# Optimization experiments

Measured on AMD Instinct MI355X. Metric: run time of the kernel, lower is better.

The kernel has to match this reference:

```python
import jax, jax.numpy as jnp
import numpy as np

DIM = 2048
HID = 4096          # multiple_of*ceil(int(2*6144/3)/256)
STATE = 128
HEADS = 64
GROUPS = 1
CONV = 4
CHUNK = 256
HEAD_DIM = HID // HEADS            # 64
CONV_DIM = HID + 2 * GROUPS * STATE  # 4352
D_IN = 2 * HID + 2 * GROUPS * STATE + HEADS  # 8512


def setup_inputs() -> dict:
    key = jax.random.key(0)
    ks = jax.random.split(key, 8)
    x = jax.random.normal(ks[0], (1, 4096, DIM), dtype=jnp.float32)
    in_proj_w = jax.random.normal(ks[1], (D_IN, DIM), jnp.float32) * (DIM ** -0.5)
    conv_w = jax.random.normal(ks[2], (CONV_DIM, CONV), jnp.float32) * (CONV ** -0.5)
    # dt_bias init: log(expm1(uniform(dt_min, dt_max)))
    dt_bias = jnp.log(jnp.expm1(jax.random.uniform(ks[3], (HEADS,), jnp.float32, 0.001, 0.1)))
    # A_log init: log(uniform(A_init_min, A_init_max))
    A_log = jnp.log(jax.random.uniform(ks[4], (HEADS,), jnp.float32, 1.0, 16.0))
    D = jnp.ones((HEADS,), jnp.float32)
    norm_w = jnp.ones((HID,), jnp.float32)
    out_proj_w = jax.random.normal(ks[5], (DIM, HID), jnp.float32) * (HID ** -0.5)
    return dict(x=x, in_proj_w=in_proj_w, conv_w=conv_w, dt_bias=dt_bias,
                A_log=A_log, D=D, norm_w=norm_w, out_proj_w=out_proj_w)


def _causal_conv1d_silu(xBC, w):
    # xBC: (b, s, c); w: (c, k) depthwise causal conv, then SiLU
    b, s, c = xBC.shape
    k = w.shape[1]
    xp = jnp.pad(xBC, ((0, 0), (k - 1, 0), (0, 0)))
    out = xp[:, 0:s, :] * w[:, 0]
    for i in range(1, k):
        out = out + xp[:, i:i + s, :] * w[:, i]
    return jax.nn.silu(out)


def _ssd_chunk_scan(x, dt, A, B, C, D, chunk):
    # x: (b,s,h,p), dt: (b,s,h) post-softplus, A: (h,) negative, B,C: (b,s,g,n)
    b, s, h, p = x.shape
    g, n = B.shape[2], B.shape[3]
    c = s // chunk
    Bh = jnp.repeat(B, h // g, axis=2).reshape(b, c, chunk, h, n)
    Ch = jnp.repeat(C, h // g, axis=2).reshape(b, c, chunk, h, n)
    xr = x.reshape(b, c, chunk, h, p)
    dtr = dt.reshape(b, c, chunk, h)
    dA = dtr * A                      # (b,c,l,h)
    dAc = jnp.cumsum(dA, axis=2)      # (b,c,l,h)
    # intra-chunk (diagonal blocks): decay[i,j] = exp(dAc[i]-dAc[j]) for i>=j
    seg = dAc[:, :, :, None, :] - dAc[:, :, None, :, :]   # (b,c,l,l,h)
    mask = jnp.tril(jnp.ones((chunk, chunk), bool))
    Lmat = jnp.where(mask[None, None, :, :, None], jnp.exp(seg), 0.0)
    xdt = xr * dtr[..., None]         # dt-scaled inputs
    y_diag = jnp.einsum('bclhn,bcshn,bclsh,bcshp->bclhp', Ch, Bh, Lmat, xdt)
    # per-chunk end states
    dA_last = dAc[:, :, -1:, :]                       # (b,c,1,h)
    decay_states = jnp.exp(dA_last - dAc)             # (b,c,l,h)
    states = jnp.einsum('bclhn,bclh,bclhp->bchpn', Bh, decay_states, xdt)
    # inter-chunk recurrence
    chunk_decay = jnp.exp(dA_last[:, :, 0, :])        # (b,c,h)
    def step(carry, inp):
        dec, st = inp
        new = carry * dec[:, :, None, None] + st
        return new, carry
    init = jnp.zeros((b, h, p, n), x.dtype)
    _, prev = jax.lax.scan(step, init,
                           (jnp.moveaxis(chunk_decay, 1, 0), jnp.moveaxis(states, 1, 0)))
    prev = jnp.moveaxis(prev, 0, 1)                   # (b,c,h,p,n) state entering each chunk
    y_off = jnp.einsum('bclhn,bclh,bchpn->bclhp', Ch, jnp.exp(dAc), prev)
    y = (y_diag + y_off).reshape(b, s, h, p)
    return y + x * D[None, None, :, None]


def reference(x, in_proj_w, conv_w, dt_bias, A_log, D, norm_w, out_proj_w):
    b, s, _ = x.shape
    zxbcdt = x @ in_proj_w.T                          # (b,s,D_IN)
    z = zxbcdt[..., :HID]
    xBC = zxbcdt[..., HID:HID + CONV_DIM]
    dt = zxbcdt[..., HID + CONV_DIM:]                 # (b,s,heads)
    xBC = _causal_conv1d_silu(xBC, conv_w)
    xh = xBC[..., :HID].reshape(b, s, HEADS, HEAD_DIM)
    B = xBC[..., HID:HID + GROUPS * STATE].reshape(b, s, GROUPS, STATE)
    C = xBC[..., HID + GROUPS * STATE:].reshape(b, s, GROUPS, STATE)
    A = -jnp.exp(A_log)
    dt = jax.nn.softplus(dt + dt_bias)                # dt_softplus=True with dt_bias
    y = _ssd_chunk_scan(xh, dt, A, B, C, D, CHUNK)
    y = y.reshape(b, s, HID)
    y = y * jax.nn.silu(z)                            # gated
    y = y * jax.lax.rsqrt(jnp.mean(y * y, axis=-1, keepdims=True) + 1e-5) * norm_w
    return y @ out_proj_w.T
```

## Files before the change

### kernel.cpp

```cpp
#include <hip/hip_runtime.h>
#include <cstdint>
#include <cstddef>

#define SEQ      4096
#define DIMIN    2048
#define HID      4096
#define STATE    128
#define HEADS    64
#define HEAD_DIM 64
#define CONV_DIM 4352
#define D_IN     8512
#define WROWS    8576
#define XBCD_N   4480
#define CHUNK    256
#define NCHUNK   16

typedef __attribute__((ext_vector_type(8))) short short8;
typedef __attribute__((ext_vector_type(4))) float floatx4;
typedef __attribute__((ext_vector_type(4))) unsigned int uintx4;

__device__ __forceinline__ unsigned short f2bf(float f) {
    union { float f; unsigned int u; } v; v.f = f;
    unsigned int r = v.u + 0x7FFFu + ((v.u >> 16) & 1u);
    return (unsigned short)(r >> 16);
}
__device__ __forceinline__ float bf2f(unsigned short u) {
    union { unsigned int u; float f; } v; v.u = ((unsigned int)u) << 16;
    return v.f;
}

__global__ void k_convert(const float* __restrict__ src, unsigned short* __restrict__ dst,
                          long n, long nsrc) {
    long i = (long)blockIdx.x * blockDim.x + threadIdx.x;
    if (i >= n) return;
    float v = (i < nsrc) ? src[i] : 0.f;
    dst[i] = f2bf(v);
}

#define BM 128
#define BN 128
#define BK 64
#define LDT 72

template <int BF16OUT>
__global__ __launch_bounds__(256) void k_gemm(
    const unsigned short* __restrict__ A, const unsigned short* __restrict__ B,
    void* __restrict__ Cout, int K, int ldc, float* __restrict__ aux, int auxc0)
{
    __shared__ __attribute__((aligned(16))) unsigned short As[BM * LDT];
    __shared__ __attribute__((aligned(16))) unsigned short Bs[BN * LDT];
    const int tid = threadIdx.x;
    const int bm = blockIdx.y, bn = blockIdx.x;
    const int wid = tid >> 6, lane = tid & 63;
    const int wm = (wid >> 1) * 64, wn = (wid & 1) * 64;
    const int lrow = lane & 15;
    const int lk = (lane >> 4) * 8;

    floatx4 acc[4][4];
#pragma unroll
    for (int i = 0; i < 4; ++i)
#pragma unroll
        for (int j = 0; j < 4; ++j) acc[i][j] = (floatx4){0.f, 0.f, 0.f, 0.f};

    const long a_base = (long)bm * BM * K;
    const long b_base = (long)bn * BN * K;

    for (int k0 = 0; k0 < K; k0 += BK) {
#pragma unroll
        for (int i = 0; i < 4; ++i) {
            int c = tid + i * 256;
            int row = c >> 3;
            int col = (c & 7) * 8;
            *(uintx4*)&As[row * LDT + col] = *(const uintx4*)&A[a_base + (long)row * K + k0 + col];
            *(uintx4*)&Bs[row * LDT + col] = *(const uintx4*)&B[b_base + (long)row * K + k0 + col];
        }
        __syncthreads();
#pragma unroll
        for (int kk = 0; kk < BK; kk += 32) {
            short8 af[4], bfr[4];
#pragma unroll
            for (int i = 0; i < 4; ++i)
                af[i] = *(const short8*)&As[(wm + i * 16 + lrow) * LDT + kk + lk];
#pragma unroll
            for (int j = 0; j < 4; ++j)
                bfr[j] = *(const short8*)&Bs[(wn + j * 16 + lrow) * LDT + kk + lk];
#pragma unroll
            for (int i = 0; i < 4; ++i)
#pragma unroll
                for (int j = 0; j < 4; ++j)
                    acc[i][j] = __builtin_amdgcn_mfma_f32_16x16x32_bf16(af[i], bfr[j], acc[i][j], 0, 0, 0);
        }
        __syncthreads();
    }
    const int rcol = lane & 15;
    const int rrow = (lane >> 4) * 4;
#pragma unroll
    for (int i = 0; i < 4; ++i)
#pragma unroll
        for (int j = 0; j < 4; ++j) {
            int col = bn * BN + wn + j * 16 + rcol;
#pragma unroll
            for (int r = 0; r < 4; ++r) {
                int row = bm * BM + wm + i * 16 + rrow + r;
                float v = acc[i][j][r];
                if (BF16OUT) {
                    ((unsigned short*)Cout)[(long)row * ldc + col] = f2bf(v);
                    if (aux && col >= auxc0 && col < auxc0 + 64)
                        aux[(long)row * 64 + (col - auxc0)] = v;
                } else {
                    ((float*)Cout)[(long)row * ldc + col] = v;
                }
            }
        }
}

__global__ void k_conv(const unsigned short* __restrict__ xbcd, const float* __restrict__ convw,
                       unsigned short* __restrict__ xc) {
    long i = (long)blockIdx.x * 256 + threadIdx.x;
    if (i >= (long)SEQ * CONV_DIM) return;
    int c = (int)(i % CONV_DIM);
    int s = (int)(i / CONV_DIM);
    float w0 = convw[c * 4 + 0], w1 = convw[c * 4 + 1];
    float w2 = convw[c * 4 + 2], w3 = convw[c * 4 + 3];
    float acc = bf2f(xbcd[(long)s * XBCD_N + c]) * w3;
    if (s >= 1) acc += bf2f(xbcd[(long)(s - 1) * XBCD_N + c]) * w2;
    if (s >= 2) acc += bf2f(xbcd[(long)(s - 2) * XBCD_N + c]) * w1;
    if (s >= 3) acc += bf2f(xbcd[(long)(s - 3) * XBCD_N + c]) * w0;
    float sl = acc / (1.f + __expf(-acc));
    xc[i] = f2bf(sl);
}

__global__ __launch_bounds__(256) void k_dt(const float* __restrict__ dtraw,
        const float* __restrict__ dt_bias, const float* __restrict__ A_log,
        float* __restrict__ dtv, float* __restrict__ dAc, float* __restrict__ dAlast)
{
    int c = blockIdx.x, h = blockIdx.y;
    int l = threadIdx.x;
    __shared__ float sh[CHUNK];
    float v = dtraw[(long)(c * CHUNK + l) * 64 + h] + dt_bias[h];
    float dt = (v > 20.f) ? v : log1pf(__expf(v));
    float Ah = -__expf(A_log[h]);
    float dA = dt * Ah;
    sh[l] = dA;
    __syncthreads();
    float x = dA;
#pragma unroll
    for (int off = 1; off < CHUNK; off <<= 1) {
        float t = (l >= off) ? sh[l - off] : 0.f;
        __syncthreads();
        x += t;
        sh[l] = x;
        __syncthreads();
    }
    dtv[(long)(c * CHUNK + l) * HEADS + h] = dt;
    dAc[(long)(c * CHUNK + l) * HEADS + h] = x;
    if (l == CHUNK - 1) dAlast[c * HEADS + h] = x;
}

__global__ __launch_bounds__(256) void k_G(const unsigned short* __restrict__ xc, float* __restrict__ G) {
    int c = blockIdx.x, l = blockIdx.y;
    int s = threadIdx.x;
    __shared__ float Csh[STATE];
    if (s < STATE) Csh[s] = bf2f(xc[(long)(c * CHUNK + l) * CONV_DIM + HID + STATE + s]);
    __syncthreads();
    const unsigned short* Brow = xc + (long)(c * CHUNK + s) * CONV_DIM + HID;
    float acc = 0.f;
#pragma unroll
    for (int n = 0; n < STATE; n += 8) {
        short8 b8 = *(const short8*)&Brow[n];
#pragma unroll
        for (int j = 0; j < 8; ++j)
            acc += Csh[n + j] * bf2f((unsigned short)b8[j]);
    }
    G[((long)c * CHUNK + l) * CHUNK + s] = acc;
}

__global__ __launch_bounds__(256) void k_states(
    const unsigned short* __restrict__ xc, const float* __restrict__ dtv,
    const float* __restrict__ dAc, const float* __restrict__ dAlast,
    float* __restrict__ states)
{
    int c = blockIdx.x, h = blockIdx.y;
    int t = threadIdx.x;
    __shared__ float xs[64][64];
    __shared__ float dA_sh[CHUNK], dt_sh[CHUNK];
    long base_s = (long)c * CHUNK;
    dA_sh[t] = dAc[(base_s + t) * HEADS + h];
    dt_sh[t] = dtv[(base_s + t) * HEADS + h];
    __syncthreads();
    float dAl = dAlast[c * HEADS + h];
    int p0 = t >> 5;
    int n0 = t & 31;
    float acc[8][4];
#pragma unroll
    for (int ip = 0; ip < 8; ++ip)
#pragma unroll
        for (int j = 0; j < 4; ++j) acc[ip][j] = 0.f;

    for (int lb = 0; lb < 4; ++lb) {
#pragma unroll
        for (int i = 0; i < 16; ++i) {
            int e = t + i * 256;
            int r = e >> 6, pcol = e & 63;
            float ds = __expf(dAl - dA_sh[lb * 64 + r]) * dt_sh[lb * 64 + r];
            xs[r][pcol] = bf2f(xc[(base_s + lb * 64 + r) * CONV_DIM + h * HEAD_DIM + pcol]) * ds;
        }
        __syncthreads();
        for (int lp = 0; lp < 64; ++lp) {
            const unsigned short* Brow = xc + (base_s + lb * 64 + lp) * CONV_DIM + HID;
            float bv[4];
#pragma unroll
            for (int j = 0; j < 4; ++j) bv[j] = bf2f(Brow[n0 + 32 * j]);
#pragma unroll
            for (int ip = 0; ip < 8; ++ip) {
                float xv = xs[lp][p0 + 8 * ip];
#pragma unroll
                for (int j = 0; j < 4; ++j) acc[ip][j] += xv * bv[j];
            }
        }
        __syncthreads();
    }
    float* Sb = states + (long)(c * HEADS + h) * HEAD_DIM * STATE;
#pragma unroll
    for (int ip = 0; ip < 8; ++ip)
#pragma unroll
        for (int j = 0; j < 4; ++j)
            Sb[(p0 + 8 * ip) * STATE + n0 + 32 * j] = acc[ip][j];
}

__global__ void k_scan(float* __restrict__ states, const float* __restrict__ dAlast) {
    int t = blockIdx.x * 256 + threadIdx.x;
    if (t >= HEADS * HEAD_DIM * STATE) return;
    int h = t >> 13;
    const long stride = (long)HEADS * HEAD_DIM * STATE;
    float carry = 0.f;
    for (int c = 0; c < NCHUNK; ++c) {
        float s = states[c * stride + t];
        float dec = __expf(dAlast[c * HEADS + h]);
        states[c * stride + t] = carry;
        carry = carry * dec + s;
    }
}

#define XDTS 264
#define PVS  136
__global__ __launch_bounds__(256, 3) void k_ssd_y(
    const unsigned short* __restrict__ xc, const float* __restrict__ G,
    const float* __restrict__ dtv, const float* __restrict__ dAc,
    const float* __restrict__ prev, const float* __restrict__ Dp,
    unsigned short* __restrict__ y)
{
    __shared__ __attribute__((aligned(16))) unsigned short xdtT[64 * XDTS];
    __shared__ __attribute__((aligned(16))) unsigned short pvB[64 * PVS];
    __shared__ float dA_sh[CHUNK];
    __shared__ float dt_sh[CHUNK];
    const int c = blockIdx.x, h = blockIdx.y;
    const int t = threadIdx.x;
    const int w = t >> 6, lane = t & 63;
    const long base_s = (long)c * CHUNK;

    dA_sh[t] = dAc[(base_s + t) * HEADS + h];
    dt_sh[t] = dtv[(base_s + t) * HEADS + h];
    __syncthreads();

    {
        const float* Pb = prev + (long)(c * HEADS + h) * HEAD_DIM * STATE;
#pragma unroll
        for (int i = 0; i < 32; ++i) {
            int e = t + i * 256;
            int p = e >> 7, n = e & 127;
            pvB[p * PVS + n] = f2bf(Pb[e]);
        }
    }
#pragma unroll
    for (int i = 0; i < 64; ++i) {
        int e = t + i * 256;
        int p = e & 63, s = e >> 6;
        float v = bf2f(xc[(base_s + s) * CONV_DIM + h * HEAD_DIM + p]) * dt_sh[s];
        xdtT[p * XDTS + s] = f2bf(v);
    }
    __syncthreads();

    floatx4 acc[4][4];
#pragma unroll
    for (int i = 0; i < 4; ++i)
#pragma unroll
        for (int j = 0; j < 4; ++j) acc[i][j] = (floatx4){0.f, 0.f, 0.f, 0.f};

    const int lrow = lane & 15;
    const int kgrp = (lane >> 4) * 8;
    float myA[4], eAl[4];
#pragma unroll
    for (int i = 0; i < 4; ++i) {
        int l = w * 64 + i * 16 + lrow;
        myA[i] = dA_sh[l];
        eAl[i] = __expf(myA[i]);
    }

    for (int k0 = 0; k0 < STATE; k0 += 32) {
        short8 af[4], bfr[4];
#pragma unroll
        for (int i = 0; i < 4; ++i) {
            int l = w * 64 + i * 16 + lrow;
            union { short8 v; unsigned short u[8]; } r, o;
            r.v = *(const short8*)&xc[(base_s + l) * CONV_DIM + (HID + STATE) + k0 + kgrp];
#pragma unroll
            for (int j = 0; j < 8; ++j) o.u[j] = f2bf(bf2f(r.u[j]) * eAl[i]);
            af[i] = o.v;
        }
#pragma unroll
        for (int j = 0; j < 4; ++j)
            bfr[j] = *(const short8*)&pvB[(j * 16 + lrow) * PVS + k0 + kgrp];
#pragma unroll
        for (int i = 0; i < 4; ++i)
#pragma unroll
            for (int j = 0; j < 4; ++j)
                acc[i][j] = __builtin_amdgcn_mfma_f32_16x16x32_bf16(af[i], bfr[j], acc[i][j], 0, 0, 0);
    }

    for (int k0 = 0; k0 < (w + 1) * 64; k0 += 32) {
        short8 af[4], bfr[4];
#pragma unroll
        for (int i = 0; i < 4; ++i) {
            int l = w * 64 + i * 16 + lrow;
            const float* Gp = G + (base_s + l) * (long)CHUNK + k0 + kgrp;
            float4 g0 = *(const float4*)Gp;
            float4 g1 = *(const float4*)(Gp + 4);
            float ga[8] = {g0.x, g0.y, g0.z, g0.w, g1.x, g1.y, g1.z, g1.w};
            union { short8 v; unsigned short u[8]; } o;
#pragma unroll
            for (int j = 0; j < 8; ++j) {
                int s = k0 + kgrp + j;
                float e = __expf(fminf(myA[i] - dA_sh[s], 0.f));
                float m = (s <= l) ? ga[j] * e : 0.f;
                o.u[j] = f2bf(m);
            }
            af[i] = o.v;
        }
#pragma unroll
        for (int j = 0; j < 4; ++j)
            bfr[j] = *(const short8*)&xdtT[(j * 16 + lrow) * XDTS + k0 + kgrp];
#pragma unroll
        for (int i = 0; i < 4; ++i)
#pragma unroll
            for (int j = 0; j < 4; ++j)
                acc[i][j] = __builtin_amdgcn_mfma_f32_16x16x32_bf16(af[i], bfr[j], acc[i][j], 0, 0, 0);
    }

    const float Dh = Dp[h];
    const int rrow = (lane >> 4) * 4;
#pragma unroll
    for (int i = 0; i < 4; ++i)
#pragma unroll
        for (int j = 0; j < 4; ++j) {
            int p = j * 16 + lrow;
#pragma unroll
            for (int r = 0; r < 4; ++r) {
                int l = w * 64 + i * 16 + rrow + r;
                float v = acc[i][j][r] + Dh * bf2f(xc[(base_s + l) * CONV_DIM + h * HEAD_DIM + p]);
                y[(base_s + l) * (long)HID + h * HEAD_DIM + p] = f2bf(v);
            }
        }
}

__global__ __launch_bounds__(256) void k_norm(
    const unsigned short* __restrict__ y, const unsigned short* __restrict__ z,
    const float* __restrict__ norm_w, unsigned short* __restrict__ yb)
{
    int s = blockIdx.x;
    int t = threadIdx.x;
    const unsigned short* yrow = y + (long)s * HID;
    const unsigned short* zrow = z + (long)s * HID;
    float vals[16];
    float ss = 0.f;
#pragma unroll
    for (int i = 0; i < 16; ++i) {
        int j = t + i * 256;
        float yv = bf2f(yrow[j]);
        float zv = bf2f(zrow[j]);
        float g = yv * (zv / (1.f + __expf(-zv)));
        vals[i] = g;
        ss += g * g;
    }
#pragma unroll
    for (int off = 32; off > 0; off >>= 1) ss += __shfl_down(ss, off);
    __shared__ float wsum[4];
    int lane = t & 63, wid = t >> 6;
    if (lane == 0) wsum[wid] = ss;
    __syncthreads();
    float total = wsum[0] + wsum[1] + wsum[2] + wsum[3];
    float scale = rsqrtf(total / HID + 1e-5f);
#pragma unroll
    for (int i = 0; i < 16; ++i) {
        int j = t + i * 256;
        yb[(long)s * HID + j] = f2bf(vals[i] * scale * norm_w[j]);
    }
}

extern "C" void kernel_launch(void* const* d_in, const int* in_sizes, int n_in,
                              void* d_out, int out_size, void* d_ws, size_t ws_size,
                              hipStream_t stream) {
    const float* x          = (const float*)d_in[0];
    const float* in_proj_w  = (const float*)d_in[1];
    const float* conv_w     = (const float*)d_in[2];
    const float* dt_bias    = (const float*)d_in[3];
    const float* A_log      = (const float*)d_in[4];
    const float* Dp         = (const float*)d_in[5];
    const float* norm_w     = (const float*)d_in[6];
    const float* out_proj_w = (const float*)d_in[7];
    char* ws = (char*)d_ws;

    const size_t off_xb    = 0;
    const size_t off_wbin  = off_xb    + (size_t)SEQ * DIMIN * 2;
    const size_t off_xbcd  = off_wbin  + (size_t)WROWS * DIMIN * 2;
    const size_t off_xc    = off_xbcd  + (size_t)SEQ * XBCD_N * 2;
    const size_t off_dtraw = off_xc    + (size_t)SEQ * CONV_DIM * 2;
    const size_t off_dtv   = off_dtraw + (size_t)SEQ * 64 * 4;
    const size_t off_dAc   = off_dtv   + (size_t)SEQ * HEADS * 4;
    const size_t off_dAl   = off_dAc   + (size_t)SEQ * HEADS * 4;
    const size_t off_G     = off_dAl   + (size_t)NCHUNK * HEADS * 4;
    const size_t needed    = off_G     + (size_t)NCHUNK * CHUNK * CHUNK * 4;
    if (ws_size < needed) return;

    unsigned short* xb    = (unsigned short*)(ws + off_xb);
    unsigned short* wbin  = (unsigned short*)(ws + off_wbin);
    unsigned short* xbcd  = (unsigned short*)(ws + off_xbcd);
    unsigned short* xc    = (unsigned short*)(ws + off_xc);
    float* dtraw = (float*)(ws + off_dtraw);
    float* dtv   = (float*)(ws + off_dtv);
    float* dAc   = (float*)(ws + off_dAc);
    float* dAl   = (float*)(ws + off_dAl);
    float* G     = (float*)(ws + off_G);

    float* states      = (float*)d_out;
    unsigned short* z  = (unsigned short*)d_out;
    unsigned short* y  = xbcd;
    unsigned short* yb = xc;
    unsigned short* wob = wbin;

    { long n = (long)SEQ * DIMIN;
      k_convert<<<(unsigned)((n + 255) / 256), 256, 0, stream>>>(x, xb, n, n); }
    { long n = (long)WROWS * DIMIN, nsrc = (long)D_IN * DIMIN;
      k_convert<<<(unsigned)((n + 255) / 256), 256, 0, stream>>>(in_proj_w, wbin, n, nsrc); }
    k_gemm<1><<<dim3(XBCD_N / BN, SEQ / BM), 256, 0, stream>>>(
        xb, wbin + (size_t)HID * DIMIN, (void*)xbcd, DIMIN, XBCD_N, dtraw, 4352);
    { long n = (long)SEQ * CONV_DIM;
      k_conv<<<(unsigned)((n + 255) / 256), 256, 0, stream>>>(xbcd, conv_w, xc); }
    k_dt<<<dim3(NCHUNK, HEADS), 256, 0, stream>>>(dtraw, dt_bias, A_log, dtv, dAc, dAl);
    k_G<<<dim3(NCHUNK, CHUNK), 256, 0, stream>>>(xc, G);
    k_states<<<dim3(NCHUNK, HEADS), 256, 0, stream>>>(xc, dtv, dAc, dAl, states);
    k_scan<<<(HEADS * HEAD_DIM * STATE) / 256, 256, 0, stream>>>(states, dAl);
    k_ssd_y<<<dim3(NCHUNK, HEADS), 256, 0, stream>>>(xc, G, dtv, dAc, states, Dp, y);
    k_gemm<1><<<dim3(HID / BN, SEQ / BM), 256, 0, stream>>>(
        xb, wbin, (void*)z, DIMIN, HID, nullptr, 0);
    k_norm<<<SEQ, 256, 0, stream>>>(y, z, norm_w, yb);
    { long n = (long)DIMIN * HID;
      k_convert<<<(unsigned)((n + 255) / 256), 256, 0, stream>>>(out_proj_w, wob, n, n); }
    k_gemm<0><<<dim3(DIMIN / BN, SEQ / BM), 256, 0, stream>>>(
        yb, wob, d_out, HID, DIMIN, nullptr, 0);
}
```

Baseline: 783.5 us.

## Use direct global-to-LDS loads with XOR swizzle and grouped tile order in GEMM

The GEMM tile loads now go straight from global memory into LDS through the global_load_lds builtin, so they no longer pass through registers. Because that path writes each wave's lanes contiguously, the padded LDS layout is replaced by an unpadded one with an XOR swizzle on the 16-byte groups to avoid bank conflicts. Block indices are also remapped into groups of 8 column tiles to improve L2 reuse. It is still a single-buffered loop with a sync after loading, so no overlap is added, and the swizzle index math must match the builtin's per-lane placement exactly.

Result: faster. 762.2 us (-2.7%).

```diff
diff --git a/kernel.cpp b/kernel.cpp
--- a/kernel.cpp
+++ b/kernel.cpp
@@ -19,6 +19,12 @@
 typedef __attribute__((ext_vector_type(4))) float floatx4;
 typedef __attribute__((ext_vector_type(4))) unsigned int uintx4;
 
+#define AS1 __attribute__((address_space(1)))
+#define AS3 __attribute__((address_space(3)))
+__device__ __forceinline__ void gload_lds16(const void* g, void* l) {
+    __builtin_amdgcn_global_load_lds((const AS1 unsigned int*)g, (AS3 unsigned int*)l, 16, 0, 0);
+}
+
 __device__ __forceinline__ unsigned short f2bf(float f) {
     union { float f; unsigned int u; } v; v.f = f;
     unsigned int r = v.u + 0x7FFFu + ((v.u >> 16) & 1u);
@@ -40,21 +46,31 @@
 #define BM 128
 #define BN 128
 #define BK 64
-#define LDT 72
 
 template <int BF16OUT>
 __global__ __launch_bounds__(256) void k_gemm(
     const unsigned short* __restrict__ A, const unsigned short* __restrict__ B,
     void* __restrict__ Cout, int K, int ldc, float* __restrict__ aux, int auxc0)
 {
-    __shared__ __attribute__((aligned(16))) unsigned short As[BM * LDT];
-    __shared__ __attribute__((aligned(16))) unsigned short Bs[BN * LDT];
+    __shared__ __attribute__((aligned(16))) unsigned short As[BM * BK];
+    __shared__ __attribute__((aligned(16))) unsigned short Bs[BN * BK];
     const int tid = threadIdx.x;
-    const int bm = blockIdx.y, bn = blockIdx.x;
+
+    const int GN = 8;
+    const int nbx = gridDim.x, nby = gridDim.y;
+    int flat = blockIdx.y * nbx + blockIdx.x;
+    int group = flat / (GN * nby);
+    int gw = min(GN, nbx - group * GN);
+    int rem = flat - group * (GN * nby);
+    int bn = group * GN + rem % gw;
+    int bm = rem / gw;
+
     const int wid = tid >> 6, lane = tid & 63;
     const int wm = (wid >> 1) * 64, wn = (wid & 1) * 64;
     const int lrow = lane & 15;
-    const int lk = (lane >> 4) * 8;
+    const int gk = lane >> 4;
+    const int srow = lane >> 3;
+    const int sgrp = (lane & 7) ^ (lane >> 3);
 
     floatx4 acc[4][4];
 #pragma unroll
@@ -66,24 +82,25 @@
     const long b_base = (long)bn * BN * K;
 
     for (int k0 = 0; k0 < K; k0 += BK) {
+        const unsigned short* Ak = A + a_base + k0;
+        const unsigned short* Bk = B + b_base + k0;
 #pragma unroll
         for (int i = 0; i < 4; ++i) {
-            int c = tid + i * 256;
-            int row = c >> 3;
-            int col = (c & 7) * 8;
-            *(uintx4*)&As[row * LDT + col] = *(const uintx4*)&A[a_base + (long)row * K + k0 + col];
-            *(uintx4*)&Bs[row * LDT + col] = *(const uintx4*)&B[b_base + (long)row * K + k0 + col];
+            int rbase = wid * 32 + i * 8;
+            gload_lds16(Ak + (long)(rbase + srow) * K + sgrp * 8, &As[rbase * BK]);
+            gload_lds16(Bk + (long)(rbase + srow) * K + sgrp * 8, &Bs[rbase * BK]);
         }
         __syncthreads();
 #pragma unroll
         for (int kk = 0; kk < BK; kk += 32) {
+            const int slot8 = (((kk >> 3) + gk) ^ (lrow & 7)) * 8;
             short8 af[4], bfr[4];
 #pragma unroll
             for (int i = 0; i < 4; ++i)
-                af[i] = *(const short8*)&As[(wm + i * 16 + lrow) * LDT + kk + lk];
+                af[i] = *(const short8*)&As[(wm + i * 16 + lrow) * BK + slot8];
 #pragma unroll
             for (int j = 0; j < 4; ++j)
-                bfr[j] = *(const short8*)&Bs[(wn + j * 16 + lrow) * LDT + kk + lk];
+                bfr[j] = *(const short8*)&Bs[(wn + j * 16 + lrow) * BK + slot8];
 #pragma unroll
             for (int i = 0; i < 4; ++i)
 #pragma unroll
```
